# Kernel optimization log

Hardware: AMD Instinct MI355X
Metric: run time of the kernel (lower is better)

## Reference

```python
import jax, jax.numpy as jnp
import numpy as np

EPS = 1e-5

def conv2d(x, w, b=None, pad=0):
    y = jax.lax.conv_general_dilated(x, w, (1, 1), [(pad, pad), (pad, pad)],
                                     dimension_numbers=('NCHW', 'OIHW', 'NCHW'))
    if b is not None:
        y = y + b[None, :, None, None]
    return y

def bn(x, w, b, m, v):
    scale = w / jnp.sqrt(v + EPS)
    return x * scale[None, :, None, None] + (b - m * scale)[None, :, None, None]

def setup_inputs() -> dict:
    key = jax.random.key(0)
    ks = jax.random.split(key, 24)
    B, Cin, H, W = 4, 2048, 60, 60
    Ci = Cin // 4           # inter_channels = 512
    Cq = Ci // 8            # q/k dim = 64
    Cout = 59
    r = lambda k, s, sc=0.05: jax.random.normal(k, s, jnp.float32) * sc
    return {
        'x': jax.random.normal(ks[0], (B, Cin, H, W), jnp.float32),
        'dep': jax.random.uniform(ks[1], (B, 1, H, W), jnp.float32),
        'w5a': r(ks[2], (Ci, Cin, 3, 3)),
        'bn1_w': jax.random.uniform(ks[3], (Ci,), jnp.float32, 0.5, 1.5),
        'bn1_b': r(ks[4], (Ci,)),
        'bn1_m': r(ks[5], (Ci,)),
        'bn1_v': jax.random.uniform(ks[6], (Ci,), jnp.float32, 0.5, 1.5),
        'wq': r(ks[7], (Cq, Ci, 1, 1)), 'bq': r(ks[8], (Cq,)),
        'wk': r(ks[9], (Cq, Ci, 1, 1)), 'bk': r(ks[10], (Cq,)),
        'wv': r(ks[11], (Ci, Ci, 1, 1)), 'bv': r(ks[12], (Ci,)),
        'gamma': r(ks[13], (1,), 0.5),
        'lamb1': r(ks[14], (1,), 0.5),
        'w51': r(ks[15], (Ci, Ci, 3, 3)),
        'bn2_w': jax.random.uniform(ks[16], (Ci,), jnp.float32, 0.5, 1.5),
        'bn2_b': r(ks[17], (Ci,)),
        'bn2_m': r(ks[18], (Ci,)),
        'bn2_v': jax.random.uniform(ks[19], (Ci,), jnp.float32, 0.5, 1.5),
        'w6': r(ks[20], (Cout, Ci, 1, 1)), 'b6': r(ks[21], (Cout,)),
    }

def reference(x, dep, w5a, bn1_w, bn1_b, bn1_m, bn1_v, wq, bq, wk, bk, wv, bv,
              gamma, lamb1, w51, bn2_w, bn2_b, bn2_m, bn2_v, w6, b6):
    # conv5a: 3x3 conv -> BN (inference) -> ReLU
    f1 = jax.nn.relu(bn(conv2d(x, w5a, pad=1), bn1_w, bn1_b, bn1_m, bn1_v))
    B, C, H, W = f1.shape
    N = H * W
    q = conv2d(f1, wq, bq).reshape(B, -1, N)     # [B, C/8, N]
    k = conv2d(f1, wk, bk).reshape(B, -1, N)     # [B, C/8, N]
    v = conv2d(f1, wv, bv).reshape(B, C, N)      # [B, C, N]
    energy = jnp.einsum('bci,bcj->bij', q, k)    # [B, N, N]
    d1 = dep.reshape(B, 1, N)
    d = jnp.transpose(d1, (0, 2, 1)) - d1        # [B, N, N] depth difference
    sim = energy - lamb1[0] * jnp.square(d)      # dep_order == 2
    attn = jax.nn.softmax(sim, axis=-1)
    # out[b,c,i] = sum_j v[b,c,j] * attn[b,i,j]  (bmm with attn^T)
    out = jnp.einsum('bcj,bij->bci', v, attn).reshape(B, C, H, W)
    sa = gamma[0] * out + f1
    sc = jax.nn.relu(bn(conv2d(sa, w51, pad=1), bn2_w, bn2_b, bn2_m, bn2_v))
    # Dropout2d in eval mode is identity
    logits = conv2d(sc, w6, b6)
    return (logits,)
```

## Files before the change

### kernel.cpp

```cpp
#include <hip/hip_runtime.h>
#include <math.h>

typedef unsigned short u16;
typedef short s16x8 __attribute__((ext_vector_type(8)));
typedef float f32x4 __attribute__((ext_vector_type(4)));

#define HW 3600
#define WID 60
#define SIMS 3616
#define AROWS 3712
#define SP 4216
#define PCIN 2048

__device__ __forceinline__ u16 f2bf(float f){
  unsigned u = __float_as_uint(f);
  unsigned r = (u + 0x7fffu + ((u>>16)&1u)) >> 16;
  return (u16)r;
}
__device__ __forceinline__ float bf2f(u16 b){ return __uint_as_float(((unsigned)b)<<16); }

__device__ __forceinline__ void gl2lds16(const void* g, void* l){
  __builtin_amdgcn_global_load_lds((const __attribute__((address_space(1))) unsigned*)g,
                                   (__attribute__((address_space(3))) unsigned*)l, 16, 0, 0);
}

__device__ __forceinline__ float4 ldg4(const float* __restrict__ p){
  return *reinterpret_cast<const float4*>(p);
}

__global__ void bn_prep(const float* __restrict__ w1, const float* __restrict__ b1,
                        const float* __restrict__ m1, const float* __restrict__ v1,
                        const float* __restrict__ w2, const float* __restrict__ b2,
                        const float* __restrict__ m2, const float* __restrict__ v2,
                        float* __restrict__ sc1, float* __restrict__ sh1,
                        float* __restrict__ sc2, float* __restrict__ sh2){
  int i = threadIdx.x;
  if(i < 512){
    float s1 = w1[i] / sqrtf(v1[i] + 1e-5f);
    sc1[i] = s1; sh1[i] = b1[i] - m1[i]*s1;
    float s2 = w2[i] / sqrtf(v2[i] + 1e-5f);
    sc2[i] = s2; sh2[i] = b2[i] - m2[i]*s2;
  }
}

__global__ __launch_bounds__(256) void pack_x(const float* __restrict__ x, u16* __restrict__ xpadT){
  __shared__ float tile[64][65];
  const int b = blockIdx.z, sp0 = blockIdx.x*64, ci0 = blockIdx.y*64;
  const int t = threadIdx.x, tc = t & 63, tr = t >> 6;
  const float* xb = x + ((size_t)b*PCIN + ci0)*HW;
  #pragma unroll
  for(int l=0;l<16;l++){
    int ci = tr + l*4;
    int sp = sp0 + tc;
    float v = 0.f;
    if(sp < SP){
      int j = sp / 68, c = sp - j*68;
      int jj = j-1, cc = c-1;
      if((unsigned)jj < 60u && (unsigned)cc < 60u) v = xb[(size_t)ci*HW + jj*60 + cc];
    }
    tile[ci][tc] = v;
  }
  __syncthreads();
  const size_t PL = (size_t)4*SP*PCIN;
  u16* outb = xpadT + (size_t)b*SP*PCIN;
  #pragma unroll
  for(int l=0;l<16;l++){
    int spr = tr + l*4;
    int sp = sp0 + spr;
    if(sp < SP){
      float v = tile[tc][spr];
      u16 hh = f2bf(v);
      u16 ll = f2bf(v - bf2f(hh));
      size_t o = (size_t)sp*PCIN + ci0 + tc;
      outb[o] = hh;
      outb[o + PL] = ll;
    }
  }
}

__global__ __launch_bounds__(256) void pack_w5a(const float* __restrict__ w, u16* __restrict__ out){
  const int ci = blockIdx.x*256 + threadIdx.x;
  const int m  = blockIdx.y;
  const int rs = blockIdx.z;
  float v = w[((size_t)m*PCIN + ci)*9 + rs];
  u16 hh = f2bf(v);
  u16 ll = f2bf(v - bf2f(hh));
  size_t base = ((size_t)rs*512 + m)*6144;
  out[base + ci]        = hh;
  out[base + 2048 + ci] = ll;
  out[base + 4096 + ci] = hh;
}

__global__ __launch_bounds__(256) void pack_w51(const float* __restrict__ w, u16* __restrict__ out){
  const int ci = blockIdx.x*256 + threadIdx.x;
  const int m  = blockIdx.y;
  const int rs = blockIdx.z;
  float v = w[((size_t)m*512 + ci)*9 + rs];
  out[((size_t)rs*512 + m)*512 + ci] = f2bf(v);
}

template<int MODE>
__global__ __launch_bounds__(512) void mfma_gemm(
    const u16* __restrict__ A, const u16* __restrict__ B,
    const float* __restrict__ scale, const float* __restrict__ shift,
    const float* __restrict__ f1, const float* __restrict__ gamma,
    float* __restrict__ outF, u16* __restrict__ outH)
{
  constexpr int CIC = (MODE==0)? 2048 : 512;
  constexpr int KRS = (MODE==0)? 6144 : 512;
  constexpr int KPR = KRS/32;
  constexpr int NSTEP = (MODE==2)? (SIMS/32) : (9*KPR);
  constexpr int NTA = (MODE==2)? 116 : 120;
  constexpr int NB  = (MODE==2)? 29  : 30;

  __shared__ __align__(16) u16 lds[3*8192];

  const int t  = threadIdx.x;

  const int wg = blockIdx.x;
  const int chunk = (4*NTA) >> 3;
  const int wgid = (wg & 7) * chunk + (wg >> 3);
  const int mt = wgid / NTA;
  const int nt = wgid - mt*NTA;
  const int m0 = mt << 7;
  const int b  = nt / NB;
  const int nb = nt - b*NB;

  const int srow = t & 127;
  const int skc  = t >> 7;

  const u16* Abase;
  if constexpr(MODE==2) Abase = A + (size_t)b*512*SIMS + (size_t)(m0+srow)*SIMS + skc*8;
  else                  Abase = A + (size_t)(m0+srow)*KRS + skc*8;

  const u16* Bbase;
  if constexpr(MODE==2){
    Bbase = B + (size_t)b*AROWS*SIMS + (size_t)(nb*128 + srow)*SIMS + skc*8;
  } else {
    int seg = srow >> 6, wl = srow & 63;
    int spb = (nb*2 + seg)*68 + wl;
    Bbase = B + (size_t)b*SP*CIC + (size_t)spb*CIC + skc*8;
  }
  const size_t PL = (size_t)4*SP*PCIN;

  f32x4 acc[4][2];
  #pragma unroll
  for(int i=0;i<4;i++)
    #pragma unroll
    for(int j=0;j<2;j++) acc[i][j] = (f32x4){0.f,0.f,0.f,0.f};

  const int lane = t & 63;
  const int wv = t >> 6;
  const int wm = (wv >> 2) << 6;
  const int wn = (wv & 3) << 5;
  const int fr = lane & 15, fq = lane >> 4;
  const char* ldsc = (const char*)lds;
  const int aoff = fq*2048 + (wm+fr)*16;
  const int boff = 8192 + fq*2048 + (wn+fr)*16;

  auto stage = [&](int st, int q){
    int rs = 0, k0;
    if constexpr(MODE==2){ k0 = st << 5; }
    else { rs = st / KPR; k0 = (st - rs*KPR) << 5; }
    const u16* ga;
    if constexpr(MODE==2) ga = Abase + k0;
    else                  ga = Abase + (size_t)rs*512*KRS + k0;
    gl2lds16(ga, &lds[(size_t)q*8192 + t*8]);
    const u16* gb;
    if constexpr(MODE==2){ gb = Bbase + k0; }
    else {
      int r = rs/3, s = rs - r*3;
      int plane = (MODE==0)? (k0 >> 12) : 0;
      int ci0 = k0 & (CIC-1);
      gb = Bbase + (size_t)plane*PL + (size_t)(r*68 + s)*CIC + ci0;
    }
    gl2lds16(gb, &lds[(size_t)q*8192 + 4096 + t*8]);
  };

  auto compute = [&](int q){
    const char* base = ldsc + q*16384;
    s16x8 af[4], bg[2];
    #pragma unroll
    for(int i=0;i<4;i++) af[i] = *(const s16x8*)(base + aoff + i*256);
    #pragma unroll
    for(int j=0;j<2;j++) bg[j] = *(const s16x8*)(base + boff + j*256);
    __builtin_amdgcn_s_setprio(1);
    #pragma unroll
    for(int i=0;i<4;i++)
      #pragma unroll
      for(int j=0;j<2;j++)
        acc[i][j] = __builtin_amdgcn_mfma_f32_16x16x32_bf16(af[i], bg[j], acc[i][j], 0,0,0);
    __builtin_amdgcn_s_setprio(0);
  };

  stage(0, 0);
  stage(1, 1);
  int cur = 0;
  for(int st = 0; st < NSTEP-2; ++st){
    int q2 = cur + 2; if(q2 >= 3) q2 -= 3;
    stage(st+2, q2);
    asm volatile("s_waitcnt vmcnt(4)" ::: "memory");
    __builtin_amdgcn_s_barrier();
    asm volatile("" ::: "memory");
    compute(cur);
    asm volatile("" ::: "memory");
    __builtin_amdgcn_s_barrier();
    asm volatile("" ::: "memory");
    cur = (cur+1 == 3)? 0 : cur+1;
  }
  asm volatile("s_waitcnt vmcnt(2)" ::: "memory");
  __builtin_amdgcn_s_barrier();
  asm volatile("" ::: "memory");
  compute(cur);
  cur = (cur+1 == 3)? 0 : cur+1;
  asm volatile("s_waitcnt vmcnt(0)" ::: "memory");
  __builtin_amdgcn_s_barrier();
  asm volatile("" ::: "memory");
  compute(cur);

  if constexpr(MODE==0 || MODE==1){
    #pragma unroll
    for(int i=0;i<4;i++){
      #pragma unroll
      for(int q=0;q<4;q++){
        int m = m0 + wm + i*16 + fq*4 + q;
        float scl = scale[m], shf = shift[m];
        #pragma unroll
        for(int j=0;j<2;j++){
          int np = nb*128 + wn + j*16 + fr;
          int h = np>>6, w = np&63;
          if(w < 60){
            float v = fmaxf(fmaf(acc[i][j][q], scl, shf), 0.f);
            size_t o = ((size_t)b*512 + m)*HW + h*60 + w;
            if constexpr(MODE==0) outF[o] = v;
            else                  outH[o] = f2bf(v);
          }
        }
      }
    }
  } else {
    float g = gamma[0];
    #pragma unroll
    for(int j=0;j<2;j++){
      int ip = nb*128 + wn + j*16 + fr;
      if(ip < HW){
        int h = ip/60, w = ip - h*60;
        size_t spo = (size_t)b*SP*512 + (size_t)((h+1)*68 + (w+1))*512;
        #pragma unroll
        for(int i=0;i<4;i++){
          #pragma unroll
          for(int q=0;q<4;q++){
            int m = m0 + wm + i*16 + fq*4 + q;
            float v = fmaf(g, acc[i][j][q], f1[((size_t)b*512 + m)*HW + ip]);
            outH[spo + m] = f2bf(v);
          }
        }
      }
    }
  }
}

template<bool INBF, bool GM, bool OUTBF>
__global__ __launch_bounds__(256) void gemm1x1(const void* __restrict__ inv,
    const float* __restrict__ w, const float* __restrict__ bias,
    float* __restrict__ outF, u16* __restrict__ outH, int M, int K, int OS)
{
  const int b  = blockIdx.z;
  const int m0 = blockIdx.x * 64;
  const int n0 = blockIdx.y * 64;
  const int t  = threadIdx.x;
  const int tm = t >> 4, tn = t & 15;

  __shared__ __align__(16) float As[16][64];
  __shared__ __align__(16) float Bs[16][64];

  float acc[4][4] = {};

  const int arow = t >> 2, acol = (t & 3) << 2;
  const int bkk  = t & 15, bnl  = (t >> 4) << 2;
  const bool bvalid = (n0 + bnl) < HW;

  for(int k0 = 0; k0 < K; k0 += 16){
    float4 av = make_float4(0.f,0.f,0.f,0.f);
    if(!GM || (m0 + arow) < M)
      av = ldg4(&w[(size_t)(m0 + arow)*K + k0 + acol]);
    As[acol+0][arow] = av.x;
    As[acol+1][arow] = av.y;
    As[acol+2][arow] = av.z;
    As[acol+3][arow] = av.w;

    float4 bv = make_float4(0.f,0.f,0.f,0.f);
    if(bvalid){
      if constexpr(INBF){
        const u16* inb = (const u16*)inv + (size_t)b*K*HW;
        const u16* p = &inb[(size_t)(k0 + bkk)*HW + n0 + bnl];
        bv.x = bf2f(p[0]); bv.y = bf2f(p[1]); bv.z = bf2f(p[2]); bv.w = bf2f(p[3]);
      } else {
        const float* inb = (const float*)inv + (size_t)b*K*HW;
        bv = ldg4(&inb[(size_t)(k0 + bkk)*HW + n0 + bnl]);
      }
    }
    *reinterpret_cast<float4*>(&Bs[bkk][bnl]) = bv;

    __syncthreads();
    #pragma unroll
    for(int kk=0;kk<16;kk++){
      float4 a  = *reinterpret_cast<const float4*>(&As[kk][tm<<2]);
      float4 bb = *reinterpret_cast<const float4*>(&Bs[kk][tn<<2]);
      float ar[4] = {a.x,a.y,a.z,a.w};
      float br[4] = {bb.x,bb.y,bb.z,bb.w};
      #pragma unroll
      for(int ii=0;ii<4;ii++)
        #pragma unroll
        for(int jj=0;jj<4;jj++)
          acc[ii][jj] = fmaf(ar[ii], br[jj], acc[ii][jj]);
    }
    __syncthreads();
  }

  int n = n0 + (tn<<2);
  if(n < OS){
    #pragma unroll
    for(int ii=0;ii<4;ii++){
      int m = m0 + (tm<<2) + ii;
      if(!GM || m < M){
        float bi = bias[m];
        #pragma unroll
        for(int jj=0;jj<4;jj++){
          int nn = n + jj;
          float val = (nn < HW) ? (acc[ii][jj] + bi) : 0.f;
          if constexpr(OUTBF) outH[((size_t)b*M + m)*OS + nn] = f2bf(val);
          else                outF[((size_t)b*M + m)*OS + nn] = val;
        }
      }
    }
  }
}

__global__ __launch_bounds__(256) void energy_sim(
    const float* __restrict__ q, const float* __restrict__ kptr,
    const float* __restrict__ dep, const float* __restrict__ lamb1,
    float* __restrict__ sim)
{
  const int i0 = blockIdx.y * 64;
  const int j0 = blockIdx.x * 64;
  const int t  = threadIdx.x;
  const int tm = t >> 4, tn = t & 15;

  __shared__ __align__(16) float Qs[64][64];
  __shared__ __align__(16) float Ks[64][64];

  {
    const int cc = t >> 4;
    const int il = (t & 15) << 2;
    #pragma unroll
    for(int it=0; it<4; it++){
      int c = cc + it*16;
      float4 qv = make_float4(0.f,0.f,0.f,0.f);
      float4 kv = make_float4(0.f,0.f,0.f,0.f);
      if(i0 + il < HW) qv = ldg4(&q[(size_t)c*HW + i0 + il]);
      if(j0 + il < HW) kv = ldg4(&kptr[(size_t)c*HW + j0 + il]);
      *reinterpret_cast<float4*>(&Qs[c][il]) = qv;
      *reinterpret_cast<float4*>(&Ks[c][il]) = kv;
    }
  }
  __syncthreads();

  float acc[4][4] = {};
  #pragma unroll 4
  for(int c=0;c<64;c++){
    float4 a  = *reinterpret_cast<const float4*>(&Qs[c][tm<<2]);
    float4 bv = *reinterpret_cast<const float4*>(&Ks[c][tn<<2]);
    float ar[4] = {a.x,a.y,a.z,a.w};
    float br[4] = {bv.x,bv.y,bv.z,bv.w};
    #pragma unroll
    for(int ii=0;ii<4;ii++)
      #pragma unroll
      for(int jj=0;jj<4;jj++)
        acc[ii][jj] = fmaf(ar[ii], br[jj], acc[ii][jj]);
  }

  float lam = lamb1[0];
  float di[4], dj[4];
  #pragma unroll
  for(int ii=0;ii<4;ii++){ int i = i0+(tm<<2)+ii; di[ii] = (i<HW)? dep[i] : 0.f; }
  #pragma unroll
  for(int jj=0;jj<4;jj++){ int j = j0+(tn<<2)+jj; dj[jj] = (j<HW)? dep[j] : 0.f; }

  int j = j0 + (tn<<2);
  if(j < HW){
    #pragma unroll
    for(int ii=0;ii<4;ii++){
      int i = i0 + (tm<<2) + ii;
      if(i < HW){
        float4 o;
        float d0 = di[ii]-dj[0]; o.x = acc[ii][0] - lam*d0*d0;
        float d1 = di[ii]-dj[1]; o.y = acc[ii][1] - lam*d1*d1;
        float d2 = di[ii]-dj[2]; o.z = acc[ii][2] - lam*d2*d2;
        float d3 = di[ii]-dj[3]; o.w = acc[ii][3] - lam*d3*d3;
        *reinterpret_cast<float4*>(&sim[(size_t)i*SIMS + j]) = o;
      }
    }
  }
}

__global__ __launch_bounds__(256) void softmax_attn(const float* __restrict__ sim,
                                                    u16* __restrict__ attn){
  __shared__ float redM[4], redS[4];
  const int row = blockIdx.x;
  const float* p = sim + (size_t)row*SIMS;
  u16*   a = attn + (size_t)row*SIMS;
  const int wid = threadIdx.x >> 6, lane = threadIdx.x & 63;

  float m = -3.4e38f, s = 0.f;
  for(int j=threadIdx.x; j<HW; j+=256){
    float v = p[j];
    float mo = m;
    m = fmaxf(m, v);
    s = s*__expf(mo - m) + __expf(v - m);
  }
  #pragma unroll
  for(int o=32;o>0;o>>=1){
    float m2 = __shfl_xor(m, o, 64);
    float s2 = __shfl_xor(s, o, 64);
    float mn = fmaxf(m, m2);
    s = s*__expf(m - mn) + s2*__expf(m2 - mn);
    m = mn;
  }
  if(lane==0){ redM[wid] = m; redS[wid] = s; }
  __syncthreads();
  float M = fmaxf(fmaxf(redM[0],redM[1]), fmaxf(redM[2],redM[3]));
  float S = redS[0]*__expf(redM[0]-M) + redS[1]*__expf(redM[1]-M)
          + redS[2]*__expf(redM[2]-M) + redS[3]*__expf(redM[3]-M);
  float inv = 1.0f / S;
  for(int j=threadIdx.x; j<HW; j+=256) a[j] = f2bf(__expf(p[j]-M) * inv);
  if(threadIdx.x < SIMS-HW) a[HW + threadIdx.x] = 0;
}

extern "C" void kernel_launch(void* const* d_in, const int* in_sizes, int n_in,
                              void* d_out, int out_size, void* d_ws, size_t ws_size,
                              hipStream_t stream)
{
  const float* x    = (const float*)d_in[0];
  const float* dep  = (const float*)d_in[1];
  const float* w5a  = (const float*)d_in[2];
  const float* bn1w = (const float*)d_in[3];
  const float* bn1b = (const float*)d_in[4];
  const float* bn1m = (const float*)d_in[5];
  const float* bn1v = (const float*)d_in[6];
  const float* wq   = (const float*)d_in[7];
  const float* bq   = (const float*)d_in[8];
  const float* wk   = (const float*)d_in[9];
  const float* bk   = (const float*)d_in[10];
  const float* wv   = (const float*)d_in[11];
  const float* bv   = (const float*)d_in[12];
  const float* gamma= (const float*)d_in[13];
  const float* lamb1= (const float*)d_in[14];
  const float* w51  = (const float*)d_in[15];
  const float* bn2w = (const float*)d_in[16];
  const float* bn2b = (const float*)d_in[17];
  const float* bn2m = (const float*)d_in[18];
  const float* bn2v = (const float*)d_in[19];
  const float* w6   = (const float*)d_in[20];
  const float* b6   = (const float*)d_in[21];
  float* out = (float*)d_out;

  char* cur = (char*)d_ws;
  auto alloc = [&](size_t bytes)->char*{ char* p = cur; cur += (bytes + 255) & ~(size_t)255; return p; };

  float* sc1 = (float*)alloc(512*4);
  float* sh1 = (float*)alloc(512*4);
  float* sc2 = (float*)alloc(512*4);
  float* sh2 = (float*)alloc(512*4);
  u16* xpadT = (u16*)alloc((size_t)2*4*SP*PCIN*2);
  u16* W5ab  = (u16*)alloc((size_t)9*512*6144*2);
  u16* W51b  = (u16*)alloc((size_t)9*512*512*2);
  float* f1  = (float*)alloc((size_t)4*512*HW*4);
  float* qb  = (float*)alloc((size_t)4*64*HW*4);
  float* kb  = (float*)alloc((size_t)4*64*HW*4);
  u16* vb    = (u16*)alloc((size_t)4*512*SIMS*2);
  float* sim = (float*)alloc((size_t)HW*SIMS*4);
  u16* attn  = (u16*)alloc((size_t)4*AROWS*SIMS*2);
  u16* sapadT= (u16*)alloc((size_t)4*SP*512*2);
  u16* scb   = (u16*)alloc((size_t)4*512*HW*2);

  bn_prep<<<1, 512, 0, stream>>>(bn1w,bn1b,bn1m,bn1v, bn2w,bn2b,bn2m,bn2v,
                                 sc1,sh1,sc2,sh2);

  hipMemsetAsync(sapadT, 0, (size_t)4*SP*512*2, stream);

  pack_x  <<<dim3(66,32,4), 256, 0, stream>>>(x, xpadT);
  pack_w5a<<<dim3(8,512,9), 256, 0, stream>>>(w5a, W5ab);
  pack_w51<<<dim3(2,512,9), 256, 0, stream>>>(w51, W51b);

  mfma_gemm<0><<<480, 512, 0, stream>>>(W5ab, xpadT, sc1, sh1,
                                        nullptr, nullptr, f1, nullptr);

  gemm1x1<false,false,false><<<dim3(1,57,4), 256, 0, stream>>>(f1, wq, bq, qb, nullptr, 64, 512, HW);
  gemm1x1<false,false,false><<<dim3(1,57,4), 256, 0, stream>>>(f1, wk, bk, kb, nullptr, 64, 512, HW);
  gemm1x1<false,false,true ><<<dim3(8,57,4), 256, 0, stream>>>(f1, wv, bv, nullptr, vb, 512, 512, SIMS);

  for(int b=0;b<4;b++){
    energy_sim<<<dim3(57,57), 256, 0, stream>>>(qb + (size_t)b*64*HW,
                                                kb + (size_t)b*64*HW,
                                                dep + (size_t)b*HW, lamb1, sim);
    softmax_attn<<<HW, 256, 0, stream>>>(sim, attn + (size_t)b*AROWS*SIMS);
  }

  mfma_gemm<2><<<464, 512, 0, stream>>>(vb, attn, nullptr, nullptr,
                                        f1, gamma, nullptr, sapadT);

  mfma_gemm<1><<<480, 512, 0, stream>>>(W51b, sapadT, sc2, sh2,
                                        nullptr, nullptr, nullptr, scb);

  gemm1x1<true,true,false><<<dim3(1,57,4), 256, 0, stream>>>(scb, w6, b6, out, nullptr, 59, 512, HW);
}
```

Measured before the change: 3.242 ms.

## Use 256-thread MFMA GEMM blocks with 64x64 per-wave tiles and new LDS layout

Restructures the shared MFMA GEMM so each block uses 4 waves instead of 8, with each wave computing a 64x64 output tile (4x4 MFMA fragments) rather than 64x32. The global-to-LDS staging is reorganised so each thread issues two A and two B loads per stage into a fragment-friendly LDS layout, and the wait counts are adjusted to match. This raises register-level reuse of LDS fragments per MFMA and halves the thread count per block, at the cost of more accumulator registers and possibly lower latency hiding.

```diff
diff --git a/kernel.cpp b/kernel.cpp
--- a/kernel.cpp
+++ b/kernel.cpp
@@ -100,7 +100,7 @@
 }
 
 template<int MODE>
-__global__ __launch_bounds__(512) void mfma_gemm(
+__global__ __launch_bounds__(256) void mfma_gemm(
     const u16* __restrict__ A, const u16* __restrict__ B,
     const float* __restrict__ scale, const float* __restrict__ shift,
     const float* __restrict__ f1, const float* __restrict__ gamma,
@@ -110,85 +110,88 @@
   constexpr int KRS = (MODE==0)? 6144 : 512;
   constexpr int KPR = KRS/32;
   constexpr int NSTEP = (MODE==2)? (SIMS/32) : (9*KPR);
-  constexpr int NTA = (MODE==2)? 116 : 120;
-  constexpr int NB  = (MODE==2)? 29  : 30;
+  constexpr int NB  = (MODE==2)? 29 : 30;
+  constexpr int GCHUNK = (16*NB) >> 3;
 
   __shared__ __align__(16) u16 lds[3*8192];
 
   const int t  = threadIdx.x;
 
   const int wg = blockIdx.x;
-  const int chunk = (4*NTA) >> 3;
-  const int wgid = (wg & 7) * chunk + (wg >> 3);
-  const int mt = wgid / NTA;
-  const int nt = wgid - mt*NTA;
+  const int wgid = (wg & 7)*GCHUNK + (wg >> 3);
+  const int mt = wgid / (4*NB);
+  const int nt = wgid - mt*(4*NB);
   const int m0 = mt << 7;
   const int b  = nt / NB;
   const int nb = nt - b*NB;
 
-  const int srow = t & 127;
-  const int skc  = t >> 7;
-
-  const u16* Abase;
-  if constexpr(MODE==2) Abase = A + (size_t)b*512*SIMS + (size_t)(m0+srow)*SIMS + skc*8;
-  else                  Abase = A + (size_t)(m0+srow)*KRS + skc*8;
-
-  const u16* Bbase;
-  if constexpr(MODE==2){
-    Bbase = B + (size_t)b*AROWS*SIMS + (size_t)(nb*128 + srow)*SIMS + skc*8;
-  } else {
-    int seg = srow >> 6, wl = srow & 63;
-    int spb = (nb*2 + seg)*68 + wl;
-    Bbase = B + (size_t)b*SP*CIC + (size_t)spb*CIC + skc*8;
+  const int rowA = ((t>>6)<<4) + (t&15);
+  const int chnk = (t>>4)&3;
+
+  const u16* Ap[2]; const u16* Bp[2];
+  #pragma unroll
+  for(int p=0;p<2;p++){
+    int r = rowA + p*64;
+    if constexpr(MODE==2) Ap[p] = A + (size_t)b*512*SIMS + (size_t)(m0+r)*SIMS + chnk*8;
+    else                  Ap[p] = A + (size_t)(m0+r)*KRS + chnk*8;
+    if constexpr(MODE==2){
+      Bp[p] = B + (size_t)b*AROWS*SIMS + (size_t)(nb*128 + r)*SIMS + chnk*8;
+    } else {
+      int spb = (nb*2 + p)*68 + rowA;
+      Bp[p] = B + (size_t)b*SP*CIC + (size_t)spb*CIC + chnk*8;
+    }
   }
   const size_t PL = (size_t)4*SP*PCIN;
 
-  f32x4 acc[4][2];
+  f32x4 acc[4][4];
   #pragma unroll
   for(int i=0;i<4;i++)
     #pragma unroll
-    for(int j=0;j<2;j++) acc[i][j] = (f32x4){0.f,0.f,0.f,0.f};
+    for(int j=0;j<4;j++) acc[i][j] = (f32x4){0.f,0.f,0.f,0.f};
 
   const int lane = t & 63;
   const int wv = t >> 6;
-  const int wm = (wv >> 2) << 6;
-  const int wn = (wv & 3) << 5;
+  const int wm = (wv >> 1) << 6;
+  const int wn = (wv & 1) << 6;
   const int fr = lane & 15, fq = lane >> 4;
   const char* ldsc = (const char*)lds;
-  const int aoff = fq*2048 + (wm+fr)*16;
-  const int boff = 8192 + fq*2048 + (wn+fr)*16;
+  const int abase = (wm >> 4)*1024 + fq*256 + fr*16;
+  const int bbase = 8192 + (wn >> 4)*1024 + fq*256 + fr*16;
 
   auto stage = [&](int st, int q){
     int rs = 0, k0;
     if constexpr(MODE==2){ k0 = st << 5; }
     else { rs = st / KPR; k0 = (st - rs*KPR) << 5; }
-    const u16* ga;
-    if constexpr(MODE==2) ga = Abase + k0;
-    else                  ga = Abase + (size_t)rs*512*KRS + k0;
-    gl2lds16(ga, &lds[(size_t)q*8192 + t*8]);
-    const u16* gb;
-    if constexpr(MODE==2){ gb = Bbase + k0; }
+    size_t aoffg; size_t boffg;
+    int plane = 0, ci0 = 0, rsh = 0;
+    if constexpr(MODE==2){ aoffg = k0; boffg = k0; }
     else {
-      int r = rs/3, s = rs - r*3;
-      int plane = (MODE==0)? (k0 >> 12) : 0;
-      int ci0 = k0 & (CIC-1);
-      gb = Bbase + (size_t)plane*PL + (size_t)(r*68 + s)*CIC + ci0;
-    }
-    gl2lds16(gb, &lds[(size_t)q*8192 + 4096 + t*8]);
+      aoffg = (size_t)rs*512*KRS + k0;
+      int r3 = rs/3, s3 = rs - r3*3;
+      plane = (MODE==0)? (k0 >> 12) : 0;
+      ci0 = k0 & (CIC-1);
+      boffg = (size_t)plane*PL + (size_t)(r3*68 + s3)*CIC + ci0;
+    }
+    u16* lb = &lds[q*8192];
+    #pragma unroll
+    for(int p=0;p<2;p++){
+      gl2lds16(Ap[p] + aoffg, lb + p*2048 + t*8);
+      gl2lds16(Bp[p] + boffg, lb + 4096 + p*2048 + t*8);
+    }
   };
 
   auto compute = [&](int q){
     const char* base = ldsc + q*16384;
-    s16x8 af[4], bg[2];
-    #pragma unroll
-    for(int i=0;i<4;i++) af[i] = *(const s16x8*)(base + aoff + i*256);
-    #pragma unroll
-    for(int j=0;j<2;j++) bg[j] = *(const s16x8*)(base + boff + j*256);
+    s16x8 af[4], bg[4];
+    #pragma unroll
+    for(int i=0;i<4;i++) af[i] = *(const s16x8*)(base + abase + i*1024);
+    #pragma unroll
+    for(int j=0;j<4;j++) bg[j] = *(const s16x8*)(base + bbase + j*1024);
     __builtin_amdgcn_s_setprio(1);
     #pragma unroll
     for(int i=0;i<4;i++)
       #pragma unroll
-      for(int j=0;j<2;j++)
+      for(int j=0;j<4;j++)
         acc[i][j] = __builtin_amdgcn_mfma_f32_16x16x32_bf16(af[i], bg[j], acc[i][j], 0,0,0);
     __builtin_amdgcn_s_setprio(0);
   };
@@ -199,7 +202,7 @@
   for(int st = 0; st < NSTEP-2; ++st){
     int q2 = cur + 2; if(q2 >= 3) q2 -= 3;
     stage(st+2, q2);
-    asm volatile("s_waitcnt vmcnt(4)" ::: "memory");
+    asm volatile("s_waitcnt vmcnt(8)" ::: "memory");
     __builtin_amdgcn_s_barrier();
     asm volatile("" ::: "memory");
     compute(cur);
@@ -208,7 +211,7 @@
     asm volatile("" ::: "memory");
     cur = (cur+1 == 3)? 0 : cur+1;
   }
-  asm volatile("s_waitcnt vmcnt(2)" ::: "memory");
+  asm volatile("s_waitcnt vmcnt(4)" ::: "memory");
   __builtin_amdgcn_s_barrier();
   asm volatile("" ::: "memory");
   compute(cur);
@@ -226,7 +229,7 @@
         int m = m0 + wm + i*16 + fq*4 + q;
         float scl = scale[m], shf = shift[m];
         #pragma unroll
-        for(int j=0;j<2;j++){
+        for(int j=0;j<4;j++){
           int np = nb*128 + wn + j*16 + fr;
           int h = np>>6, w = np&63;
           if(w < 60){
@@ -241,7 +244,7 @@
   } else {
     float g = gamma[0];
     #pragma unroll
-    for(int j=0;j<2;j++){
+    for(int j=0;j<4;j++){
       int ip = nb*128 + wn + j*16 + fr;
       if(ip < HW){
         int h = ip/60, w = ip - h*60;
@@ -493,7 +496,7 @@
   pack_w5a<<<dim3(8,512,9), 256, 0, stream>>>(w5a, W5ab);
   pack_w51<<<dim3(2,512,9), 256, 0, stream>>>(w51, W51b);
 
-  mfma_gemm<0><<<480, 512, 0, stream>>>(W5ab, xpadT, sc1, sh1,
+  mfma_gemm<0><<<480, 256, 0, stream>>>(W5ab, xpadT, sc1, sh1,
                                         nullptr, nullptr, f1, nullptr);
 
   gemm1x1<false,false,false><<<dim3(1,57,4), 256, 0, stream>>>(f1, wq, bq, qb, nullptr, 64, 512, HW);
@@ -507,10 +510,10 @@
     softmax_attn<<<HW, 256, 0, stream>>>(sim, attn + (size_t)b*AROWS*SIMS);
   }
 
-  mfma_gemm<2><<<464, 512, 0, stream>>>(vb, attn, nullptr, nullptr,
+  mfma_gemm<2><<<464, 256, 0, stream>>>(vb, attn, nullptr, nullptr,
                                         f1, gamma, nullptr, sapadT);
 
-  mfma_gemm<1><<<480, 512, 0, stream>>>(W51b, sapadT, sc2, sh2,
+  mfma_gemm<1><<<480, 256, 0, stream>>>(W51b, sapadT, sc2, sh2,
                                         nullptr, nullptr, nullptr, scb);
 
   gemm1x1<true,true,false><<<dim3(1,57,4), 256, 0, stream>>>(scb, w6, b6, out, nullptr, 59, 512, HW);
```

Result: faster. 2.642 ms (-18.5%).
